# Performance work log

Measured on AMD Instinct MI355X. Metric: run time of the kernel, lower is better.

Reference implementation:

```python
import jax, jax.numpy as jnp
from jax import lax
import numpy as np
import math

B, C, Hs, Ws = 2, 512, 48, 48
HW = Hs * Ws            # 2304; also m (compress_ratio = 1)
M = HW
GROUPS = 256
GS = M // GROUPS        # 9, exact split
ALPHA = 0.05
MAXITER = 43
TOL = B * HW * 1e-7     # torch: z0.numel()*tol with z0 of shape [N, HW]
EPS = 1e-5
POWER_ITERS = 100


def _make_A():
    # random projection: num_ones = round(sqrt(m)) ones per column, rows L2-normalized
    rng = np.random.RandomState(0)
    num_ones = int(round(math.sqrt(M)))  # 48
    A = np.zeros((M, HW), dtype=np.float32)
    rows = np.argsort(rng.rand(HW, M), axis=1)[:, :num_ones]  # [HW, num_ones]
    A[rows.ravel(), np.repeat(np.arange(HW), num_ones)] = 1.0
    A /= np.maximum(np.sqrt((A ** 2).sum(axis=1, keepdims=True)), 1e-12)
    return jnp.asarray(A)


def setup_inputs() -> dict:
    key = jax.random.key(0)
    ks = jax.random.split(key, 10)
    f32 = jnp.float32
    d = {
        'content': jax.random.normal(ks[0], (B, C, Hs, Ws), f32),
        'style': jax.random.normal(ks[1], (B, C, Hs, Ws), f32),
        'content_key': jax.random.normal(ks[2], (B, C, Hs, Ws), f32),
        'style_key': jax.random.normal(ks[3], (B, C, Hs, Ws), f32),
        'f_w': jax.random.normal(ks[4], (C, C), f32) * 0.02,
        'f_b': jnp.zeros((C,), f32),
        'g_w': jax.random.normal(ks[5], (C, C), f32) * 0.02,
        'g_b': jnp.zeros((C,), f32),
        'h_w': jax.random.normal(ks[6], (C, C), f32) * 0.02,
        'h_b': jnp.zeros((C,), f32),
        'A': _make_A(),
    }
    return d


def _conv1x1(x, w, b):
    # nn.Conv2d(Cin, Cout, 1): [b,c,h,w] x [o,c] + bias
    return jnp.einsum('bchw,oc->bohw', x, w) + b[None, :, None, None]


def _softshrink(x, lam):
    return jnp.sign(x) * jnp.maximum(jnp.abs(x) - lam, 0.0)


def _forward(content, style, content_key, style_key, f_w, f_b, g_w, g_b, h_w, h_b, A):
    Fq = _conv1x1(content_key, f_w, f_b).reshape(B, C, HW).transpose(0, 2, 1)  # [b,HWc,Ck]
    G = _conv1x1(style_key, g_w, g_b).reshape(B, C, HW)                        # [b,Ck,HWs]
    Hh = _conv1x1(style, h_w, h_b).reshape(B, C, HW)
    # HW <= max_sample: no subsampling branch
    style_flat = Hh.transpose(0, 2, 1)                                         # [b,HWs,C]
    S = jax.nn.softmax(jnp.einsum('bqc,bck->bqk', Fq, G), axis=-1)             # [b,HWc,HWs]
    mean = jnp.einsum('bqk,bkc->bqc', S, style_flat)                           # weighted mean
    std = jnp.sqrt(jax.nn.relu(jnp.einsum('bqk,bkc->bqc', S, style_flat ** 2) - mean ** 2))
    mean = mean.transpose(0, 2, 1)  # [b,C,HW]
    std = std.transpose(0, 2, 1)
    # random projection along spatial dim: feat @ A^T
    proj = lambda f: jnp.einsum('mh,bch->bcm', A, f)
    mean_c = proj(mean)
    std_c = proj(std)
    cont_c = proj(content.reshape(B, C, HW))
    # per-group mean/variance norm (256 equal groups of GS along compressed dim)
    g = cont_c.reshape(B, C, GROUPS, GS)
    mu = g.mean(axis=-1, keepdims=True)
    var = g.var(axis=-1, ddof=1, keepdims=True)  # torch var is unbiased
    normed = (g - mu) / jnp.sqrt(var + EPS)
    x = (normed * std_c.reshape(B, C, GROUPS, GS)
         + mean_c.reshape(B, C, GROUPS, GS)).reshape(B, C, M)
    # FISTA sparse coding: min 0.5||z A^T - x||^2 + alpha |z|_1
    Ad = lax.stop_gradient(A)
    WtW = Ad.T @ Ad
    v = jnp.full((HW,), 1.0 / math.sqrt(HW), jnp.float32)
    def _pi(v, _):
        w = WtW @ v
        return w / jnp.linalg.norm(w), None
    v, _ = lax.scan(_pi, v, None, length=POWER_ITERS)
    L = v @ (WtW @ v)  # largest eigenvalue of A^T A
    lr = 1.0 / L
    z0 = jnp.zeros((B, C, HW), x.dtype)

    def step(carry, _):
        z, y, t, done = carry
        resid = jnp.einsum('bch,mh->bcm', y, A) - x   # y @ A^T - x
        grad = jnp.einsum('bcm,mh->bch', resid, A)    # resid @ A
        zn = _softshrink(y - lr * grad, ALPHA * lr)
        diff = jnp.abs(z - zn).sum()
        tn = (1.0 + jnp.sqrt(1.0 + 4.0 * t * t)) / 2.0
        yn = zn + (t - 1.0) / tn * (zn - z)
        z2 = jnp.where(done, z, zn)
        y2 = jnp.where(done, y, yn)
        t2 = jnp.where(done, t, tn)
        done2 = done | (diff <= TOL)
        return (z2, y2, t2, done2), None

    (z, _, _, _), _ = lax.scan(step, (z0, z0, jnp.float32(1.0), jnp.array(False)),
                               None, length=MAXITER)
    return z.reshape(B, C, Hs, Ws)


def reference(content, style, content_key, style_key, f_w, f_b, g_w, g_b, h_w, h_b, A):
    return _forward(content, style, content_key, style_key,
                    f_w, f_b, g_w, g_b, h_w, h_b, A)
```

## Files before the change

kernel.cpp:

```cpp
#include <hip/hip_runtime.h>
#include <hip/hip_cooperative_groups.h>
#include <math.h>

namespace cg = cooperative_groups;

#define TPB 256

typedef _Float16 f16;
typedef _Float16 half8 __attribute__((ext_vector_type(8)));
typedef _Float16 f16x2 __attribute__((ext_vector_type(2)));
typedef _Float16 f16x4 __attribute__((ext_vector_type(4)));
typedef float floatx4 __attribute__((ext_vector_type(4)));

static constexpr int CDIM = 512;
static constexpr int HWD = 2304;
static constexpr float ALPHA = 0.05f;
static constexpr float TOLF = 4.608e-4f;

enum { EPI_F32 = 0, EPI_F16BIASN = 1, EPI_F16BIASM = 2, EPI_F16 = 3,
       EPI_WTW = 4, EPI_MEANSTD = 5 };

__device__ __forceinline__ bool fista_done(const float* __restrict__ diffArr, int iter) {
    bool done = false;
    for (int j = 0; j < iter; ++j) done = done || (diffArr[j] <= TOLF);
    return done;
}

__device__ __forceinline__ void gload_lds(const f16* g, f16* l) {
#if __has_builtin(__builtin_amdgcn_global_load_lds)
    __builtin_amdgcn_global_load_lds(
        (__attribute__((address_space(1))) void*)(g),
        (__attribute__((address_space(3))) void*)(l), 16, 0, 0);
#else
    *(int4*)l = *(const int4*)g;
#endif
}

template<int N> __device__ __forceinline__ void vwait() {
    if constexpr (N == 0)      asm volatile("s_waitcnt vmcnt(0)" ::: "memory");
    else if constexpr (N == 4) asm volatile("s_waitcnt vmcnt(4)" ::: "memory");
    else if constexpr (N == 6) asm volatile("s_waitcnt vmcnt(6)" ::: "memory");
}

__device__ __forceinline__ void barrier_f() {
    asm volatile("" ::: "memory");
    __builtin_amdgcn_s_barrier();
    asm volatile("" ::: "memory");
}

template<int EPI, int MF>
__global__ __launch_bounds__(TPB, 4) void sgemm(
    const f16* __restrict__ A, long a_bs, int lda,
    const f16* __restrict__ B, long b_bs, int ldb,
    void* __restrict__ C0, long c_bs, int ldc,
    void* __restrict__ C1,
    int K,
    const float* __restrict__ bias)
{
    constexpr int ASZ = MF * 32 * 64;
    constexpr int BSZ = 64 * 64;
    constexpr int LCNT = MF + 2;
    __shared__ alignas(16) f16 As[2 * ASZ];
    __shared__ alignas(16) f16 Bs[2 * BSZ];
    const int tid = threadIdx.x;
    const int wid = tid >> 6, lane = tid & 63;
    const int wr = wid >> 1, wc = wid & 1;

    const int gx = gridDim.x, gy = gridDim.y;
    const int nwg = gx * gy;
    const int d = blockIdx.y * gx + blockIdx.x;
    const int q = nwg >> 3, r = nwg & 7;
    const int xcd = d & 7, rest = d >> 3;
    const int wgid = (xcd < r ? xcd * (q + 1) : r * (q + 1) + (xcd - r) * q) + rest;
    const int bx = wgid / gy, by = wgid % gy;

    const int m0 = by * (MF * 32), n0 = bx << 6;
    const f16* Ab = A + (long)blockIdx.z * a_bs;
    const f16* Bb = B + (long)blockIdx.z * b_bs;

    floatx4 acc[MF][2] = {};
    floatx4 acc2[MF][2] = {};

    const int rl = lane & 15, kg = lane >> 4;
    const int lrow = lane >> 3;
    const int gs = (lane & 7) ^ lrow;
    const int nt = K >> 6;

    auto STAGE = [&](int t, int buf) {
        const long k0 = (long)t << 6;
        f16* Ad = As + buf * ASZ;
        f16* Bd = Bs + buf * BSZ;
        #pragma unroll
        for (int p = 0; p < MF; ++p) {
            const int c = wid * MF + p;
            const int R = c * 8 + lrow;
            gload_lds(Ab + (long)(m0 + R) * lda + k0 + gs * 8, Ad + c * 512);
        }
        #pragma unroll
        for (int p = 0; p < 2; ++p) {
            const int c = wid * 2 + p;
            const int R = c * 8 + lrow;
            gload_lds(Bb + (long)(n0 + R) * ldb + k0 + gs * 8, Bd + c * 512);
        }
    };

    STAGE(0, 0);
    for (int t = 0; t < nt; ++t) {
        if (t + 1 < nt) { STAGE(t + 1, (t + 1) & 1); vwait<LCNT>(); }
        else            { vwait<0>(); }
        barrier_f();
        const f16* Ac = As + (t & 1) * ASZ;
        const f16* Bc = Bs + (t & 1) * BSZ;
        #pragma unroll
        for (int kk = 0; kk < 2; ++kk) {
            const int j = kk * 4 + kg;
            half8 af[MF], bf[2];
            #pragma unroll
            for (int f = 0; f < MF; ++f) {
                const int rowa = wr * (MF * 16) + f * 16 + rl;
                af[f] = *(const half8*)&Ac[rowa * 64 + ((j ^ (rowa & 7)) * 8)];
            }
            #pragma unroll
            for (int f = 0; f < 2; ++f) {
                const int rowb = wc * 32 + f * 16 + rl;
                bf[f] = *(const half8*)&Bc[rowb * 64 + ((j ^ (rowb & 7)) * 8)];
            }
            #pragma unroll
            for (int fi = 0; fi < MF; ++fi) {
                #pragma unroll
                for (int fj = 0; fj < 2; ++fj) {
                    acc[fi][fj] = __builtin_amdgcn_mfma_f32_16x16x32_f16(af[fi], bf[fj], acc[fi][fj], 0, 0, 0);
                    if constexpr (EPI == EPI_MEANSTD) {
                        half8 bq = bf[fj] * bf[fj];
                        acc2[fi][fj] = __builtin_amdgcn_mfma_f32_16x16x32_f16(af[fi], bq, acc2[fi][fj], 0, 0, 0);
                    }
                }
            }
        }
        barrier_f();
    }

    const int rg = lane >> 4;
    const int bz = blockIdx.z;
    #pragma unroll
    for (int fi = 0; fi < MF; ++fi) {
        #pragma unroll
        for (int fj = 0; fj < 2; ++fj) {
            #pragma unroll
            for (int r2 = 0; r2 < 4; ++r2) {
                const int row = m0 + wr * (MF * 16) + fi * 16 + rg * 4 + r2;
                const int col = n0 + wc * 32 + fj * 16 + rl;
                const float v = acc[fi][fj][r2];
                if constexpr (EPI == EPI_F32) {
                    ((float*)C0)[bz * c_bs + (long)row * ldc + col] = v;
                } else if constexpr (EPI == EPI_F16BIASN) {
                    ((f16*)C0)[bz * c_bs + (long)row * ldc + col] = (f16)(v + bias[col]);
                } else if constexpr (EPI == EPI_F16BIASM) {
                    ((f16*)C0)[bz * c_bs + (long)row * ldc + col] = (f16)(v + bias[row]);
                } else if constexpr (EPI == EPI_F16) {
                    ((f16*)C0)[bz * c_bs + (long)row * ldc + col] = (f16)v;
                } else if constexpr (EPI == EPI_WTW) {
                    ((float*)C0)[(long)row * ldc + col] = v;
                    ((f16*)C1)[(long)row * ldc + col] = (f16)v;
                } else if constexpr (EPI == EPI_MEANSTD) {
                    const float m_ = v;
                    float s2 = acc2[fi][fj][r2] - m_ * m_;
                    const long o = ((long)bz * CDIM + col) * HWD + row;
                    ((f16*)C0)[o] = (f16)m_;
                    ((f16*)C1)[o] = (f16)sqrtf(s2 > 0.f ? s2 : 0.f);
                }
            }
        }
    }
}

__global__ __launch_bounds__(TPB, 3) void fista_fast(
    const f16* __restrict__ Wh,
    const float* __restrict__ xAf,
    f16* __restrict__ yA, f16* __restrict__ yB,
    const float* __restrict__ lrs,
    unsigned int* __restrict__ cnt,
    int* __restrict__ flag,
    float* __restrict__ dout)
{
    constexpr int MF = 2;
    constexpr int ASZ = MF * 32 * 64;
    constexpr int BSZ = 64 * 64;
    constexpr int LCNT = MF + 2;
    __shared__ alignas(16) f16 As[2 * ASZ];
    __shared__ alignas(16) f16 Bs[2 * BSZ];
    __shared__ float red[TPB];
    const int tid = threadIdx.x;
    const int wid = tid >> 6, lane = tid & 63;
    const int wr = wid >> 1, wc = wid & 1;

    const int d = blockIdx.x;
    const int g = d & 15;
    const int ntile = d >> 4;
    const int m0 = g << 6, n0 = ntile << 6;

    const int rl = lane & 15, kg = lane >> 4;
    const int rg = lane >> 4;
    const int lrow = lane >> 3;
    const int gs = (lane & 7) ^ lrow;
    constexpr int nt = HWD >> 6;

    const float lr = lrs[0], sh = lrs[1];

    float xar[MF][2][4], zr[MF][2][4], yr[MF][2][4];
    #pragma unroll
    for (int fi = 0; fi < MF; ++fi)
        #pragma unroll
        for (int fj = 0; fj < 2; ++fj)
            #pragma unroll
            for (int r2 = 0; r2 < 4; ++r2) {
                const int row = m0 + wr * (MF * 16) + fi * 16 + rg * 4 + r2;
                const int col = n0 + wc * 32 + fj * 16 + rl;
                xar[fi][fj][r2] = xAf[(long)row * HWD + col];
                zr[fi][fj][r2] = 0.f;
                yr[fi][fj][r2] = 0.f;
            }

    float t = 1.0f;
    for (int iter = 0; iter < 43; ++iter) {
        const float tn = (1.0f + sqrtf(1.0f + 4.0f * t * t)) * 0.5f;
        const float coef = (t - 1.0f) / tn;
        t = tn;
        const f16* Yin = (iter & 1) ? yB : yA;
        f16* Yout = (iter & 1) ? yA : yB;

        floatx4 acc[MF][2] = {};
        auto STAGE = [&](int tt, int buf) {
            const long k0 = (long)tt << 6;
            f16* Ad = As + buf * ASZ;
            f16* Bd = Bs + buf * BSZ;
            #pragma unroll
            for (int p = 0; p < MF; ++p) {
                const int c = wid * MF + p;
                const int R = c * 8 + lrow;
                gload_lds(Yin + (long)(m0 + R) * HWD + k0 + gs * 8, Ad + c * 512);
            }
            #pragma unroll
            for (int p = 0; p < 2; ++p) {
                const int c = wid * 2 + p;
                const int R = c * 8 + lrow;
                gload_lds(Wh + (long)(n0 + R) * HWD + k0 + gs * 8, Bd + c * 512);
            }
        };
        STAGE(0, 0);
        for (int tt = 0; tt < nt; ++tt) {
            if (tt + 1 < nt) { STAGE(tt + 1, (tt + 1) & 1); vwait<LCNT>(); }
            else             { vwait<0>(); }
            barrier_f();
            const f16* Ac = As + (tt & 1) * ASZ;
            const f16* Bc = Bs + (tt & 1) * BSZ;
            #pragma unroll
            for (int kk = 0; kk < 2; ++kk) {
                const int j = kk * 4 + kg;
                half8 af[MF], bf[2];
                #pragma unroll
                for (int f = 0; f < MF; ++f) {
                    const int rowa = wr * (MF * 16) + f * 16 + rl;
                    af[f] = *(const half8*)&Ac[rowa * 64 + ((j ^ (rowa & 7)) * 8)];
                }
                #pragma unroll
                for (int f = 0; f < 2; ++f) {
                    const int rowb = wc * 32 + f * 16 + rl;
                    bf[f] = *(const half8*)&Bc[rowb * 64 + ((j ^ (rowb & 7)) * 8)];
                }
                #pragma unroll
                for (int fi = 0; fi < MF; ++fi)
                    #pragma unroll
                    for (int fj = 0; fj < 2; ++fj)
                        acc[fi][fj] = __builtin_amdgcn_mfma_f32_16x16x32_f16(af[fi], bf[fj], acc[fi][fj], 0, 0, 0);
            }
            barrier_f();
        }

        float loc = 0.f;
        #pragma unroll
        for (int fi = 0; fi < MF; ++fi)
            #pragma unroll
            for (int fj = 0; fj < 2; ++fj)
                #pragma unroll
                for (int r2 = 0; r2 < 4; ++r2) {
                    const int row = m0 + wr * (MF * 16) + fi * 16 + rg * 4 + r2;
                    const int col = n0 + wc * 32 + fj * 16 + rl;
                    const float grad = acc[fi][fj][r2] - xar[fi][fj][r2];
                    const float p = yr[fi][fj][r2] - lr * grad;
                    const float ap = fabsf(p) - sh;
                    const float zn = ap > 0.f ? copysignf(ap, p) : 0.f;
                    const float zo = zr[fi][fj][r2];
                    loc += fabsf(zn - zo);
                    const float yn = zn + coef * (zn - zo);
                    zr[fi][fj][r2] = zn;
                    yr[fi][fj][r2] = yn;
                    Yout[(long)row * HWD + col] = (f16)yn;
                }
        red[tid] = loc; __syncthreads();
        for (int s = 128; s > 0; s >>= 1) { if (tid < s) red[tid] += red[tid + s]; __syncthreads(); }
        if (tid == 0 && red[0] <= TOLF)
            __hip_atomic_store(flag, 1, __ATOMIC_RELEASE, __HIP_MEMORY_SCOPE_AGENT);

        __threadfence();
        __syncthreads();
        if (tid == 0) {
            __hip_atomic_fetch_add(&cnt[g], 1u, __ATOMIC_RELEASE, __HIP_MEMORY_SCOPE_AGENT);
            const unsigned int need = 36u * (unsigned int)(iter + 1);
            while (__hip_atomic_load(&cnt[g], __ATOMIC_ACQUIRE, __HIP_MEMORY_SCOPE_AGENT) < need)
                __builtin_amdgcn_s_sleep(2);
        }
        __syncthreads();
        __threadfence();
    }

    #pragma unroll
    for (int fi = 0; fi < MF; ++fi)
        #pragma unroll
        for (int fj = 0; fj < 2; ++fj)
            #pragma unroll
            for (int r2 = 0; r2 < 4; ++r2) {
                const int row = m0 + wr * (MF * 16) + fi * 16 + rg * 4 + r2;
                const int col = n0 + wc * 32 + fj * 16 + rl;
                dout[(long)row * HWD + col] = zr[fi][fj][r2];
            }
}

__global__ __launch_bounds__(TPB, 2) void fista_coop(
    const f16* __restrict__ Wh,
    const float* __restrict__ xAf,
    f16* __restrict__ yA, f16* __restrict__ yB,
    const float* __restrict__ lrs,
    float* __restrict__ diffArr,
    const int* __restrict__ flag,
    float* __restrict__ dout)
{
    if (__hip_atomic_load(flag, __ATOMIC_ACQUIRE, __HIP_MEMORY_SCOPE_AGENT) == 0) return;
    cg::grid_group grid = cg::this_grid();
    constexpr int MF = 4;
    constexpr int ASZ = MF * 32 * 64;
    constexpr int BSZ = 64 * 64;
    constexpr int LCNT = MF + 2;
    __shared__ alignas(16) f16 As[2 * ASZ];
    __shared__ alignas(16) f16 Bs[2 * BSZ];
    __shared__ float red[TPB];
    const int tid = threadIdx.x;
    const int wid = tid >> 6, lane = tid & 63;
    const int wr = wid >> 1, wc = wid & 1;

    const int d = blockIdx.x;
    const int wgid = (d & 7) * 36 + (d >> 3);
    const int bx = wgid >> 3, by = wgid & 7;
    const int m0 = by << 7, n0 = bx << 6;

    const int rl = lane & 15, kg = lane >> 4;
    const int rg = lane >> 4;
    const int lrow = lane >> 3;
    const int gs = (lane & 7) ^ lrow;
    constexpr int nt = HWD >> 6;

    const float lr = lrs[0], sh = lrs[1];

    float xar[MF][2][4], zr[MF][2][4], yr[MF][2][4];
    #pragma unroll
    for (int fi = 0; fi < MF; ++fi)
        #pragma unroll
        for (int fj = 0; fj < 2; ++fj)
            #pragma unroll
            for (int r2 = 0; r2 < 4; ++r2) {
                const int row = m0 + wr * (MF * 16) + fi * 16 + rg * 4 + r2;
                const int col = n0 + wc * 32 + fj * 16 + rl;
                xar[fi][fj][r2] = xAf[(long)row * HWD + col];
                zr[fi][fj][r2] = 0.f;
                yr[fi][fj][r2] = 0.f;
            }

    float t = 1.0f;
    for (int iter = 0; iter < 43; ++iter) {
        const float tn = (1.0f + sqrtf(1.0f + 4.0f * t * t)) * 0.5f;
        const float coef = (t - 1.0f) / tn;
        t = tn;
        const f16* Yin = (iter & 1) ? yB : yA;
        f16* Yout = (iter & 1) ? yA : yB;

        floatx4 acc[MF][2] = {};
        auto STAGE = [&](int tt, int buf) {
            const long k0 = (long)tt << 6;
            f16* Ad = As + buf * ASZ;
            f16* Bd = Bs + buf * BSZ;
            #pragma unroll
            for (int p = 0; p < MF; ++p) {
                const int c = wid * MF + p;
                const int R = c * 8 + lrow;
                gload_lds(Yin + (long)(m0 + R) * HWD + k0 + gs * 8, Ad + c * 512);
            }
            #pragma unroll
            for (int p = 0; p < 2; ++p) {
                const int c = wid * 2 + p;
                const int R = c * 8 + lrow;
                gload_lds(Wh + (long)(n0 + R) * HWD + k0 + gs * 8, Bd + c * 512);
            }
        };
        STAGE(0, 0);
        for (int tt = 0; tt < nt; ++tt) {
            if (tt + 1 < nt) { STAGE(tt + 1, (tt + 1) & 1); vwait<LCNT>(); }
            else             { vwait<0>(); }
            barrier_f();
            const f16* Ac = As + (tt & 1) * ASZ;
            const f16* Bc = Bs + (tt & 1) * BSZ;
            #pragma unroll
            for (int kk = 0; kk < 2; ++kk) {
                const int j = kk * 4 + kg;
                half8 af[MF], bf[2];
                #pragma unroll
                for (int f = 0; f < MF; ++f) {
                    const int rowa = wr * (MF * 16) + f * 16 + rl;
                    af[f] = *(const half8*)&Ac[rowa * 64 + ((j ^ (rowa & 7)) * 8)];
                }
                #pragma unroll
                for (int f = 0; f < 2; ++f) {
                    const int rowb = wc * 32 + f * 16 + rl;
                    bf[f] = *(const half8*)&Bc[rowb * 64 + ((j ^ (rowb & 7)) * 8)];
                }
                #pragma unroll
                for (int fi = 0; fi < MF; ++fi)
                    #pragma unroll
                    for (int fj = 0; fj < 2; ++fj)
                        acc[fi][fj] = __builtin_amdgcn_mfma_f32_16x16x32_f16(af[fi], bf[fj], acc[fi][fj], 0, 0, 0);
            }
            barrier_f();
        }

        float loc = 0.f;
        #pragma unroll
        for (int fi = 0; fi < MF; ++fi)
            #pragma unroll
            for (int fj = 0; fj < 2; ++fj)
                #pragma unroll
                for (int r2 = 0; r2 < 4; ++r2) {
                    const int row = m0 + wr * (MF * 16) + fi * 16 + rg * 4 + r2;
                    const int col = n0 + wc * 32 + fj * 16 + rl;
                    const float grad = acc[fi][fj][r2] - xar[fi][fj][r2];
                    const float p = yr[fi][fj][r2] - lr * grad;
                    const float ap = fabsf(p) - sh;
                    const float zn = ap > 0.f ? copysignf(ap, p) : 0.f;
                    const float zo = zr[fi][fj][r2];
                    loc += fabsf(zn - zo);
                    const float yn = zn + coef * (zn - zo);
                    zr[fi][fj][r2] = zn;
                    yr[fi][fj][r2] = yn;
                    Yout[(long)row * HWD + col] = (f16)yn;
                }
        red[tid] = loc; __syncthreads();
        for (int s = 128; s > 0; s >>= 1) { if (tid < s) red[tid] += red[tid + s]; __syncthreads(); }
        if (tid == 0) atomicAdd(&diffArr[iter], red[0]);

        __threadfence();
        grid.sync();
        __threadfence();
        const float dsum = __hip_atomic_load(&diffArr[iter], __ATOMIC_RELAXED,
                                             __HIP_MEMORY_SCOPE_AGENT);
        if (dsum <= TOLF) break;
    }

    #pragma unroll
    for (int fi = 0; fi < MF; ++fi)
        #pragma unroll
        for (int fj = 0; fj < 2; ++fj)
            #pragma unroll
            for (int r2 = 0; r2 < 4; ++r2) {
                const int row = m0 + wr * (MF * 16) + fi * 16 + rg * 4 + r2;
                const int col = n0 + wc * 32 + fj * 16 + rl;
                dout[(long)row * HWD + col] = zr[fi][fj][r2];
            }
}

__global__ __launch_bounds__(TPB, 3) void fista_step(
    const f16* __restrict__ Yin, const f16* __restrict__ Wh,
    const float* __restrict__ xAf,
    float* __restrict__ zc, float* __restrict__ zp, f16* __restrict__ yhp,
    const float* __restrict__ lrs, float coefPrev, float coefCur,
    float* __restrict__ diffArr, int iter)
{
    if (iter > 0 && fista_done(diffArr, iter)) return;
    constexpr int MF = 2;
    constexpr int ASZ = MF * 32 * 64;
    constexpr int BSZ = 64 * 64;
    constexpr int LCNT = MF + 2;
    __shared__ alignas(16) f16 As[2 * ASZ];
    __shared__ alignas(16) f16 Bs[2 * BSZ];
    __shared__ float red[TPB];
    const int tid = threadIdx.x;
    const int wid = tid >> 6, lane = tid & 63;
    const int wr = wid >> 1, wc = wid & 1;

    const int d = blockIdx.y * gridDim.x + blockIdx.x;
    const int wgid = (d & 7) * 72 + (d >> 3);
    const int bx = wgid >> 4, by = wgid & 15;
    const int m0 = by << 6, n0 = bx << 6;

    floatx4 acc[MF][2] = {};
    const int rl = lane & 15, kg = lane >> 4;
    const int lrow = lane >> 3;
    const int gs = (lane & 7) ^ lrow;
    constexpr int nt = HWD >> 6;

    auto STAGE = [&](int t, int buf) {
        const long k0 = (long)t << 6;
        f16* Ad = As + buf * ASZ;
        f16* Bd = Bs + buf * BSZ;
        #pragma unroll
        for (int p = 0; p < MF; ++p) {
            const int c = wid * MF + p;
            const int R = c * 8 + lrow;
            gload_lds(Yin + (long)(m0 + R) * HWD + k0 + gs * 8, Ad + c * 512);
        }
        #pragma unroll
        for (int p = 0; p < 2; ++p) {
            const int c = wid * 2 + p;
            const int R = c * 8 + lrow;
            gload_lds(Wh + (long)(n0 + R) * HWD + k0 + gs * 8, Bd + c * 512);
        }
    };
    STAGE(0, 0);
    for (int t = 0; t < nt; ++t) {
        if (t + 1 < nt) { STAGE(t + 1, (t + 1) & 1); vwait<LCNT>(); }
        else            { vwait<0>(); }
        barrier_f();
        const f16* Ac = As + (t & 1) * ASZ;
        const f16* Bc = Bs + (t & 1) * BSZ;
        #pragma unroll
        for (int kk = 0; kk < 2; ++kk) {
            const int j = kk * 4 + kg;
            half8 af[MF], bf[2];
            #pragma unroll
            for (int f = 0; f < MF; ++f) {
                const int rowa = wr * (MF * 16) + f * 16 + rl;
                af[f] = *(const half8*)&Ac[rowa * 64 + ((j ^ (rowa & 7)) * 8)];
            }
            #pragma unroll
            for (int f = 0; f < 2; ++f) {
                const int rowb = wc * 32 + f * 16 + rl;
                bf[f] = *(const half8*)&Bc[rowb * 64 + ((j ^ (rowb & 7)) * 8)];
            }
            #pragma unroll
            for (int fi = 0; fi < MF; ++fi)
                #pragma unroll
                for (int fj = 0; fj < 2; ++fj)
                    acc[fi][fj] = __builtin_amdgcn_mfma_f32_16x16x32_f16(af[fi], bf[fj], acc[fi][fj], 0, 0, 0);
        }
        barrier_f();
    }

    const int rg = lane >> 4;
    const float lr = lrs[0], sh = lrs[1];
    float loc = 0.f;
    #pragma unroll
    for (int fi = 0; fi < MF; ++fi)
        #pragma unroll
        for (int fj = 0; fj < 2; ++fj)
            #pragma unroll
            for (int r2 = 0; r2 < 4; ++r2) {
                const int row = m0 + wr * (MF * 16) + fi * 16 + rg * 4 + r2;
                const int col = n0 + wc * 32 + fj * 16 + rl;
                const long off = (long)row * HWD + col;
                const float zk = zc[off];
                const float zkm = zp[off];
                const float ykf = zk + coefPrev * (zk - zkm);
                const float grad = acc[fi][fj][r2] - xAf[off];
                const float p = ykf - lr * grad;
                const float ap = fabsf(p) - sh;
                const float zn = ap > 0.f ? copysignf(ap, p) : 0.f;
                zp[off] = zn;
                yhp[off] = (f16)(zn + coefCur * (zn - zk));
                loc += fabsf(zn - zk);
            }
    red[tid] = loc; __syncthreads();
    for (int s = 128; s > 0; s >>= 1) { if (tid < s) red[tid] += red[tid + s]; __syncthreads(); }
    if (tid == 0) atomicAdd(&diffArr[iter], red[0]);
}

__global__ __launch_bounds__(TPB) void tcvt(const float* __restrict__ in, long in_bs,
                                            f16* __restrict__ out, long out_bs, int R, int Cc) {
    __shared__ float t[32][33];
    const int b = blockIdx.z;
    const int r0 = blockIdx.y << 5, c0 = blockIdx.x << 5;
    const int tx = threadIdx.x & 31, ty = threadIdx.x >> 5;
    const float* ib = in + (long)b * in_bs;
    #pragma unroll
    for (int p = 0; p < 4; ++p) {
        const int r = ty + p * 8;
        t[r][tx] = ib[(long)(r0 + r) * Cc + c0 + tx];
    }
    __syncthreads();
    f16* ob = out + (long)b * out_bs;
    #pragma unroll
    for (int p = 0; p < 4; ++p) {
        const int c = ty + p * 8;
        ob[(long)(c0 + c) * R + r0 + tx] = (f16)t[tx][c];
    }
}

__global__ void cvt16(const float4* __restrict__ in, f16x4* __restrict__ out, long n4) {
    long i = (long)blockIdx.x * blockDim.x + threadIdx.x;
    const long st = (long)gridDim.x * blockDim.x;
    for (; i < n4; i += st) {
        const float4 v = in[i];
        f16x4 o; o.x = (f16)v.x; o.y = (f16)v.y; o.z = (f16)v.z; o.w = (f16)v.w;
        out[i] = o;
    }
}

__global__ __launch_bounds__(TPB) void softmax_h(const float* __restrict__ Sf, f16* __restrict__ Sh) {
    __shared__ float row[HWD];
    __shared__ float red[TPB];
    const long base = (long)blockIdx.x * HWD;
    const int tid = threadIdx.x;
    float mx = -3.4e38f;
    for (int i = tid; i < HWD; i += TPB) { const float v = Sf[base + i]; row[i] = v; mx = fmaxf(mx, v); }
    red[tid] = mx; __syncthreads();
    for (int s = 128; s > 0; s >>= 1) { if (tid < s) red[tid] = fmaxf(red[tid], red[tid + s]); __syncthreads(); }
    mx = red[0]; __syncthreads();
    float sum = 0.f;
    for (int i = tid; i < HWD; i += TPB) { const float e = expf(row[i] - mx); row[i] = e; sum += e; }
    red[tid] = sum; __syncthreads();
    for (int s = 128; s > 0; s >>= 1) { if (tid < s) red[tid] += red[tid + s]; __syncthreads(); }
    const float inv = 1.0f / red[0];
    for (int i = tid; i < HWD; i += TPB) Sh[base + i] = (f16)(row[i] * inv);
}

__global__ __launch_bounds__(TPB) void groupnorm_x(const float* __restrict__ contc,
                                                   const float* __restrict__ meanc,
                                                   const float* __restrict__ stdc,
                                                   f16* __restrict__ xh) {
    const long base = (long)blockIdx.x * HWD + (long)threadIdx.x * 9;
    float v[9];
    float mu = 0.f;
    #pragma unroll
    for (int j = 0; j < 9; ++j) { v[j] = contc[base + j]; mu += v[j]; }
    mu *= (1.0f / 9.0f);
    float var = 0.f;
    #pragma unroll
    for (int j = 0; j < 9; ++j) { const float d = v[j] - mu; var += d * d; }
    var *= (1.0f / 8.0f);
    const float rs = 1.0f / sqrtf(var + 1e-5f);
    #pragma unroll
    for (int j = 0; j < 9; ++j)
        xh[base + j] = (f16)((v[j] - mu) * rs * (float)stdc[base + j] + (float)meanc[base + j]);
}

__global__ __launch_bounds__(TPB) void matvec_h(const f16* __restrict__ Wm,
                                                const float* __restrict__ win,
                                                float* __restrict__ wout) {
    __shared__ float red[TPB];
    const int tid = threadIdx.x;
    float s = 0.f;
    for (int i = tid; i < HWD; i += TPB) { const float v = win[i]; s += v * v; }
    red[tid] = s; __syncthreads();
    for (int st = 128; st > 0; st >>= 1) { if (tid < st) red[tid] += red[tid + st]; __syncthreads(); }
    const float ninv = rsqrtf(red[0]);
    const int row = (blockIdx.x << 2) + (tid >> 6);
    const int lane = tid & 63;
    const f16x2* wr2 = (const f16x2*)(Wm + (long)row * HWD);
    float d = 0.f;
    for (int j = lane; j < HWD / 2; j += 64) {
        const f16x2 p = wr2[j];
        d += (float)p.x * win[2 * j] + (float)p.y * win[2 * j + 1];
    }
    #pragma unroll
    for (int o = 32; o > 0; o >>= 1) d += __shfl_down(d, o);
    if (lane == 0) wout[row] = d * ninv;
}

__global__ __launch_bounds__(TPB) void kernelL(const float* __restrict__ Wf,
                                               const float* __restrict__ w,
                                               float* __restrict__ Lnum, float* __restrict__ Lden) {
    __shared__ float red[TPB];
    const int tid = threadIdx.x;
    const int row = (blockIdx.x << 2) + (tid >> 6);
    const int lane = tid & 63;
    const float* wr = Wf + (long)row * HWD;
    float d = 0.f;
    for (int j = lane; j < HWD; j += 64) d += wr[j] * w[j];
    #pragma unroll
    for (int o = 32; o > 0; o >>= 1) d += __shfl_down(d, o);
    red[tid] = (lane == 0) ? d * w[row] : 0.f;
    __syncthreads();
    for (int s = 128; s > 0; s >>= 1) { if (tid < s) red[tid] += red[tid + s]; __syncthreads(); }
    if (tid == 0) atomicAdd(Lnum, red[0]);
    if (blockIdx.x == 0) {
        __syncthreads();
        float s2 = 0.f;
        for (int i = tid; i < HWD; i += TPB) { const float v = w[i]; s2 += v * v; }
        red[tid] = s2; __syncthreads();
        for (int s = 128; s > 0; s >>= 1) { if (tid < s) red[tid] += red[tid + s]; __syncthreads(); }
        if (tid == 0) *Lden = red[0];
    }
}

__global__ void lr_fin(const float* __restrict__ Lnum, const float* __restrict__ Lden,
                       float* __restrict__ lrs) {
    const float lr = Lden[0] / Lnum[0];
    lrs[0] = lr;
    lrs[1] = ALPHA * lr;
}

__global__ void init_small(float* __restrict__ wvec, float* __restrict__ diffArr,
                           float* __restrict__ Lnum, unsigned int* __restrict__ cnt,
                           int* __restrict__ flag) {
    const int tid = threadIdx.x;
    for (int i = tid; i < HWD; i += TPB) wvec[i] = (float)(1.0 / 48.0);
    if (tid < 43) diffArr[tid] = 0.f;
    if (tid == 64) Lnum[0] = 0.f;
    if (tid >= 80 && tid < 96) cnt[tid - 80] = 0u;
    if (tid == 96) *flag = 0;
}

__global__ void zero_kernel(float4* __restrict__ p, long n4) {
    long i = (long)blockIdx.x * blockDim.x + threadIdx.x;
    const long st = (long)gridDim.x * blockDim.x;
    for (; i < n4; i += st) p[i] = make_float4(0.f, 0.f, 0.f, 0.f);
}

__global__ void zero_if(const int* __restrict__ flag, float4* __restrict__ p, long n4) {
    if (__hip_atomic_load(flag, __ATOMIC_ACQUIRE, __HIP_MEMORY_SCOPE_AGENT) == 0) return;
    long i = (long)blockIdx.x * blockDim.x + threadIdx.x;
    const long st = (long)gridDim.x * blockDim.x;
    for (; i < n4; i += st) p[i] = make_float4(0.f, 0.f, 0.f, 0.f);
}

__global__ void copy_fista(const float4* __restrict__ zfA, const float4* __restrict__ zfB,
                           float4* __restrict__ out, const float* __restrict__ diffArr, long n4) {
    int last = 42;
    for (int j = 0; j < 43; ++j) { if (diffArr[j] <= TOLF) { last = j; break; } }
    const float4* src = (last & 1) ? zfA : zfB;
    long i = (long)blockIdx.x * blockDim.x + threadIdx.x;
    const long st = (long)gridDim.x * blockDim.x;
    for (; i < n4; i += st) out[i] = src[i];
}

extern "C" void kernel_launch(void* const* d_in, const int* in_sizes, int n_in,
                              void* d_out, int out_size, void* d_ws, size_t ws_size,
                              hipStream_t stream) {
    (void)in_sizes; (void)n_in; (void)out_size;
    const float* content = (const float*)d_in[0];
    const float* style   = (const float*)d_in[1];
    const float* ckey    = (const float*)d_in[2];
    const float* skey    = (const float*)d_in[3];
    const float* f_w = (const float*)d_in[4];
    const float* f_b = (const float*)d_in[5];
    const float* g_w = (const float*)d_in[6];
    const float* g_b = (const float*)d_in[7];
    const float* h_w = (const float*)d_in[8];
    const float* h_b = (const float*)d_in[9];
    const float* Amat = (const float*)d_in[10];

    if (ws_size < 79500000) return;
    char* W = (char*)d_ws;

    const long E16 = (long)HWD * CDIM;
    const long EHH = (long)HWD * HWD;
    f16*  ckeyT = (f16*)(W + 0);
    f16*  skeyT = (f16*)(W + 4718592);
    f16*  styleT= (f16*)(W + 9437184);
    float* Sf   = (float*)(W + 0);
    f16*  Ah    = (f16*)(W + 0);
    f16*  At    = (f16*)(W + 10616832);
    f16*  Wh    = (f16*)(W + 21233664);
    f16*  W4h   = (f16*)(W + 31850496);
    f16*  W2h   = (f16*)(W + 0);
    float* contc= (float*)(W + 21233664);
    float* zfA  = (float*)(W + 0);
    float* zfB  = (float*)(W + 9437184);
    f16*  yhA   = (f16*)(W + 31850496);
    f16*  yhB   = (f16*)(W + 36569088);
    f16*  Sh    = (f16*)(W + 42467328);
    float* meanc= (float*)(W + 42467328);
    float* stdc = (float*)(W + 42467328 + 9437184);
    float* Wf   = (float*)(W + 42467328);
    float* xAf  = (float*)(W + 42467328);
    f16*  Fh    = (f16*)(W + 63700992);
    f16*  Gh    = (f16*)(W + 63700992 + 4718592);
    f16*  Hh    = (f16*)(W + 63700992 + 9437184);
    f16*  meanx = (f16*)(W + 63700992);
    f16*  stdx  = (f16*)(W + 63700992 + 4718592);
    f16*  conth = (f16*)(W + 63700992 + 9437184);
    f16*  xh    = (f16*)(W + 63700992);
    float* w_a  = (float*)(W + 77856768);
    float* w_b  = (float*)(W + 77856768 + 9216);
    float* lrs  = (float*)(W + 77856768 + 18432);
    float* Lnum = (float*)(W + 77856768 + 18440);
    float* Lden = (float*)(W + 77856768 + 18444);
    float* diffArr = (float*)(W + 77856768 + 18448);
    unsigned int* cnt = (unsigned int*)(W + 77856768 + 18624);
    int*  flag  = (int*)(W + 77856768 + 18688);
    f16*  fwh   = (f16*)(W + 77875712);
    f16*  gwh   = (f16*)(W + 77875712 + 524288);
    f16*  hwh   = (f16*)(W + 77875712 + 1048576);

    init_small<<<1, TPB, 0, stream>>>(w_a, diffArr, Lnum, cnt, flag);

    cvt16<<<256, TPB, 0, stream>>>((const float4*)f_w, (f16x4*)fwh, (long)CDIM * CDIM / 4);
    cvt16<<<256, TPB, 0, stream>>>((const float4*)g_w, (f16x4*)gwh, (long)CDIM * CDIM / 4);
    cvt16<<<256, TPB, 0, stream>>>((const float4*)h_w, (f16x4*)hwh, (long)CDIM * CDIM / 4);
    tcvt<<<dim3(72, 16, 2), TPB, 0, stream>>>(ckey, E16, ckeyT, E16, CDIM, HWD);
    tcvt<<<dim3(72, 16, 2), TPB, 0, stream>>>(skey, E16, skeyT, E16, CDIM, HWD);
    tcvt<<<dim3(72, 16, 2), TPB, 0, stream>>>(style, E16, styleT, E16, CDIM, HWD);

    sgemm<EPI_F16BIASN, 2><<<dim3(8, 36, 2), TPB, 0, stream>>>(ckeyT, E16, CDIM, fwh, 0, CDIM,
        Fh, E16, CDIM, nullptr, CDIM, f_b);
    sgemm<EPI_F16BIASN, 2><<<dim3(8, 36, 2), TPB, 0, stream>>>(skeyT, E16, CDIM, gwh, 0, CDIM,
        Gh, E16, CDIM, nullptr, CDIM, g_b);
    sgemm<EPI_F16BIASM, 2><<<dim3(36, 8, 2), TPB, 0, stream>>>(hwh, 0, CDIM, styleT, E16, CDIM,
        Hh, E16, HWD, nullptr, CDIM, h_b);

    sgemm<EPI_F32, 2><<<dim3(36, 36, 2), TPB, 0, stream>>>(Fh, E16, CDIM, Gh, E16, CDIM,
        Sf, EHH, HWD, nullptr, CDIM, nullptr);
    softmax_h<<<2 * HWD, TPB, 0, stream>>>(Sf, Sh);

    cvt16<<<2048, TPB, 0, stream>>>((const float4*)Amat, (f16x4*)Ah, EHH / 4);
    tcvt<<<dim3(72, 72, 1), TPB, 0, stream>>>(Amat, 0, At, 0, HWD, HWD);

    sgemm<EPI_MEANSTD, 2><<<dim3(8, 36, 2), TPB, 0, stream>>>(Sh, EHH, HWD, Hh, E16, HWD,
        meanx, 0, HWD, stdx, HWD, nullptr);

    cvt16<<<2048, TPB, 0, stream>>>((const float4*)content, (f16x4*)conth, (long)2 * E16 / 4);

    sgemm<EPI_F32, 2><<<dim3(36, 16, 1), TPB, 0, stream>>>(meanx, 0, HWD, Ah, 0, HWD,
        meanc, 0, HWD, nullptr, HWD, nullptr);
    sgemm<EPI_F32, 2><<<dim3(36, 16, 1), TPB, 0, stream>>>(stdx, 0, HWD, Ah, 0, HWD,
        stdc, 0, HWD, nullptr, HWD, nullptr);
    sgemm<EPI_F32, 2><<<dim3(36, 16, 1), TPB, 0, stream>>>(conth, 0, HWD, Ah, 0, HWD,
        contc, 0, HWD, nullptr, HWD, nullptr);

    groupnorm_x<<<1024, TPB, 0, stream>>>(contc, meanc, stdc, xh);

    sgemm<EPI_WTW, 2><<<dim3(36, 36, 1), TPB, 0, stream>>>(At, 0, HWD, At, 0, HWD,
        Wf, 0, HWD, Wh, HWD, nullptr);
    sgemm<EPI_F16, 2><<<dim3(36, 36, 1), TPB, 0, stream>>>(Wh, 0, HWD, Wh, 0, HWD,
        W2h, 0, HWD, nullptr, HWD, nullptr);
    sgemm<EPI_F16, 2><<<dim3(36, 36, 1), TPB, 0, stream>>>(W2h, 0, HWD, W2h, 0, HWD,
        W4h, 0, HWD, nullptr, HWD, nullptr);

    for (int it = 0; it < 25; ++it) {
        const float* win = (it & 1) ? w_b : w_a;
        float* wout = (it & 1) ? w_a : w_b;
        matvec_h<<<HWD / 4, TPB, 0, stream>>>(W4h, win, wout);
    }
    kernelL<<<HWD / 4, TPB, 0, stream>>>(Wf, w_b, Lnum, Lden);
    lr_fin<<<1, 1, 0, stream>>>(Lnum, Lden, lrs);

    sgemm<EPI_F32, 2><<<dim3(36, 16, 1), TPB, 0, stream>>>(xh, 0, HWD, At, 0, HWD,
        xAf, 0, HWD, nullptr, HWD, nullptr);

    int dev = 0; hipGetDevice(&dev);
    int coopOK = 0, numCU = 0, maxFast = 0, maxCoop = 0;
    hipDeviceGetAttribute(&coopOK, hipDeviceAttributeCooperativeLaunch, dev);
    hipDeviceGetAttribute(&numCU, hipDeviceAttributeMultiprocessorCount, dev);
    hipOccupancyMaxActiveBlocksPerMultiprocessor(&maxFast, fista_fast, TPB, 0);
    hipOccupancyMaxActiveBlocksPerMultiprocessor(&maxCoop, fista_coop, TPB, 0);
    const bool usePersist = coopOK && ((long)maxFast * numCU >= 576)
                                   && ((long)maxCoop * numCU >= 288);

    zero_kernel<<<1024, TPB, 0, stream>>>((float4*)yhA, E16 / 4);

    if (usePersist) {
        float* doutF = (float*)d_out;
        {
            void* args[] = { (void*)&Wh, (void*)&xAf, (void*)&yhA, (void*)&yhB,
                             (void*)&lrs, (void*)&cnt, (void*)&flag, (void*)&doutF };
            hipLaunchCooperativeKernel((const void*)fista_fast, dim3(576), dim3(TPB),
                                       args, 0, stream);
        }
        zero_if<<<1024, TPB, 0, stream>>>(flag, (float4*)yhA, E16 / 4);
        {
            void* args[] = { (void*)&Wh, (void*)&xAf, (void*)&yhA, (void*)&yhB,
                             (void*)&lrs, (void*)&diffArr, (void*)&flag, (void*)&doutF };
            hipLaunchCooperativeKernel((const void*)fista_coop, dim3(288), dim3(TPB),
                                       args, 0, stream);
        }
    } else {
        zero_kernel<<<1024, TPB, 0, stream>>>((float4*)zfA, E16);
        float t = 1.0f, coefPrev = 0.0f;
        for (int it = 0; it < 43; ++it) {
            const float tn = (1.0f + sqrtf(1.0f + 4.0f * t * t)) * 0.5f;
            const float coef = (t - 1.0f) / tn;
            t = tn;
            float* zc = (it & 1) ? zfB : zfA;
            float* zp = (it & 1) ? zfA : zfB;
            fista_step<<<dim3(36, 16, 1), TPB, 0, stream>>>(yhA, Wh, xAf, zc, zp, yhA,
                                                            lrs, coefPrev, coef, diffArr, it);
            coefPrev = coef;
        }
        copy_fista<<<2048, TPB, 0, stream>>>((const float4*)zfA, (const float4*)zfB,
                                             (float4*)d_out, diffArr, 2 * E16 / 4);
    }
}
```

Baseline: 2.123 ms.

## Drop device-wide fences in FISTA group barrier, relying on same-XCD L2 coherence

Removes the __threadfence calls around the per-group barrier in the persistent FISTA kernel. Y loads now use an AUX cache-policy bit so they bypass the per-CU cache, and the spin wait after the first iteration uses relaxed loads. Correctness now depends on all blocks of a group sharing one XCD's L2. On the first iteration each group records the XCC IDs of its blocks and sets the fallback flag if they span more than one. This cuts fence and cache-invalidation cost on each of the 43 iterations, but relies on the hardware placing blocks per XCD and on the flag-driven fallback path.

```diff
diff --git a/kernel.cpp b/kernel.cpp
--- a/kernel.cpp
+++ b/kernel.cpp
@@ -26,11 +26,12 @@
     return done;
 }
 
+template<int AUX>
 __device__ __forceinline__ void gload_lds(const f16* g, f16* l) {
 #if __has_builtin(__builtin_amdgcn_global_load_lds)
     __builtin_amdgcn_global_load_lds(
         (__attribute__((address_space(1))) void*)(g),
-        (__attribute__((address_space(3))) void*)(l), 16, 0, 0);
+        (__attribute__((address_space(3))) void*)(l), 16, 0, AUX);
 #else
     *(int4*)l = *(const int4*)g;
 #endif
@@ -94,13 +95,13 @@
         for (int p = 0; p < MF; ++p) {
             const int c = wid * MF + p;
             const int R = c * 8 + lrow;
-            gload_lds(Ab + (long)(m0 + R) * lda + k0 + gs * 8, Ad + c * 512);
+            gload_lds<0>(Ab + (long)(m0 + R) * lda + k0 + gs * 8, Ad + c * 512);
         }
         #pragma unroll
         for (int p = 0; p < 2; ++p) {
             const int c = wid * 2 + p;
             const int R = c * 8 + lrow;
-            gload_lds(Bb + (long)(n0 + R) * ldb + k0 + gs * 8, Bd + c * 512);
+            gload_lds<0>(Bb + (long)(n0 + R) * ldb + k0 + gs * 8, Bd + c * 512);
         }
     };
 
@@ -180,6 +181,7 @@
     f16* __restrict__ yA, f16* __restrict__ yB,
     const float* __restrict__ lrs,
     unsigned int* __restrict__ cnt,
+    unsigned int* __restrict__ xcdmask,
     int* __restrict__ flag,
     float* __restrict__ dout)
 {
@@ -199,6 +201,10 @@
     const int ntile = d >> 4;
     const int m0 = g << 6, n0 = ntile << 6;
 
+    unsigned int myxcd;
+    asm volatile("s_getreg_b32 %0, hwreg(HW_REG_XCC_ID)" : "=s"(myxcd));
+    myxcd &= 7u;
+
     const int rl = lane & 15, kg = lane >> 4;
     const int rg = lane >> 4;
     const int lrow = lane >> 3;
@@ -238,13 +244,13 @@
             for (int p = 0; p < MF; ++p) {
                 const int c = wid * MF + p;
                 const int R = c * 8 + lrow;
-                gload_lds(Yin + (long)(m0 + R) * HWD + k0 + gs * 8, Ad + c * 512);
+                gload_lds<1>(Yin + (long)(m0 + R) * HWD + k0 + gs * 8, Ad + c * 512);
             }
             #pragma unroll
             for (int p = 0; p < 2; ++p) {
                 const int c = wid * 2 + p;
                 const int R = c * 8 + lrow;
-                gload_lds(Wh + (long)(n0 + R) * HWD + k0 + gs * 8, Bd + c * 512);
+                gload_lds<0>(Wh + (long)(n0 + R) * HWD + k0 + gs * 8, Bd + c * 512);
             }
         };
         STAGE(0, 0);
@@ -302,16 +308,26 @@
         if (tid == 0 && red[0] <= TOLF)
             __hip_atomic_store(flag, 1, __ATOMIC_RELEASE, __HIP_MEMORY_SCOPE_AGENT);
 
-        __threadfence();
         __syncthreads();
         if (tid == 0) {
+            if (iter == 0)
+                __hip_atomic_fetch_or(&xcdmask[g], 1u << myxcd,
+                                      __ATOMIC_RELEASE, __HIP_MEMORY_SCOPE_AGENT);
             __hip_atomic_fetch_add(&cnt[g], 1u, __ATOMIC_RELEASE, __HIP_MEMORY_SCOPE_AGENT);
             const unsigned int need = 36u * (unsigned int)(iter + 1);
-            while (__hip_atomic_load(&cnt[g], __ATOMIC_ACQUIRE, __HIP_MEMORY_SCOPE_AGENT) < need)
-                __builtin_amdgcn_s_sleep(2);
+            if (iter == 0) {
+                while (__hip_atomic_load(&cnt[g], __ATOMIC_ACQUIRE, __HIP_MEMORY_SCOPE_AGENT) < need)
+                    __builtin_amdgcn_s_sleep(2);
+                const unsigned int m = __hip_atomic_load(&xcdmask[g], __ATOMIC_RELAXED,
+                                                         __HIP_MEMORY_SCOPE_AGENT);
+                if (__builtin_popcount(m) != 1)
+                    __hip_atomic_store(flag, 1, __ATOMIC_RELEASE, __HIP_MEMORY_SCOPE_AGENT);
+            } else {
+                while (__hip_atomic_load(&cnt[g], __ATOMIC_RELAXED, __HIP_MEMORY_SCOPE_AGENT) < need)
+                    __builtin_amdgcn_s_sleep(2);
+            }
         }
         __syncthreads();
-        __threadfence();
     }
 
     #pragma unroll
@@ -392,13 +408,13 @@
             for (int p = 0; p < MF; ++p) {
                 const int c = wid * MF + p;
                 const int R = c * 8 + lrow;
-                gload_lds(Yin + (long)(m0 + R) * HWD + k0 + gs * 8, Ad + c * 512);
+                gload_lds<0>(Yin + (long)(m0 + R) * HWD + k0 + gs * 8, Ad + c * 512);
             }
             #pragma unroll
             for (int p = 0; p < 2; ++p) {
                 const int c = wid * 2 + p;
                 const int R = c * 8 + lrow;
-                gload_lds(Wh + (long)(n0 + R) * HWD + k0 + gs * 8, Bd + c * 512);
+                gload_lds<0>(Wh + (long)(n0 + R) * HWD + k0 + gs * 8, Bd + c * 512);
             }
         };
         STAGE(0, 0);
@@ -513,13 +529,13 @@
         for (int p = 0; p < MF; ++p) {
             const int c = wid * MF + p;
             const int R = c * 8 + lrow;
-            gload_lds(Yin + (long)(m0 + R) * HWD + k0 + gs * 8, Ad + c * 512);
+            gload_lds<0>(Yin + (long)(m0 + R) * HWD + k0 + gs * 8, Ad + c * 512);
         }
         #pragma unroll
         for (int p = 0; p < 2; ++p) {
             const int c = wid * 2 + p;
             const int R = c * 8 + lrow;
-            gload_lds(Wh + (long)(n0 + R) * HWD + k0 + gs * 8, Bd + c * 512);
+            gload_lds<0>(Wh + (long)(n0 + R) * HWD + k0 + gs * 8, Bd + c * 512);
         }
     };
     STAGE(0, 0);
@@ -707,13 +723,14 @@
 
 __global__ void init_small(float* __restrict__ wvec, float* __restrict__ diffArr,
                            float* __restrict__ Lnum, unsigned int* __restrict__ cnt,
-                           int* __restrict__ flag) {
+                           unsigned int* __restrict__ xcdmask, int* __restrict__ flag) {
     const int tid = threadIdx.x;
     for (int i = tid; i < HWD; i += TPB) wvec[i] = (float)(1.0 / 48.0);
     if (tid < 43) diffArr[tid] = 0.f;
     if (tid == 64) Lnum[0] = 0.f;
     if (tid >= 80 && tid < 96) cnt[tid - 80] = 0u;
-    if (tid == 96) *flag = 0;
+    if (tid >= 96 && tid < 112) xcdmask[tid - 96] = 0u;
+    if (tid == 112) *flag = 0;
 }
 
 __global__ void zero_kernel(float4* __restrict__ p, long n4) {
@@ -793,12 +810,13 @@
     float* Lden = (float*)(W + 77856768 + 18444);
     float* diffArr = (float*)(W + 77856768 + 18448);
     unsigned int* cnt = (unsigned int*)(W + 77856768 + 18624);
-    int*  flag  = (int*)(W + 77856768 + 18688);
+    unsigned int* xcdmask = (unsigned int*)(W + 77856768 + 18688);
+    int*  flag  = (int*)(W + 77856768 + 18752);
     f16*  fwh   = (f16*)(W + 77875712);
     f16*  gwh   = (f16*)(W + 77875712 + 524288);
     f16*  hwh   = (f16*)(W + 77875712 + 1048576);
 
-    init_small<<<1, TPB, 0, stream>>>(w_a, diffArr, Lnum, cnt, flag);
+    init_small<<<1, TPB, 0, stream>>>(w_a, diffArr, Lnum, cnt, xcdmask, flag);
 
     cvt16<<<256, TPB, 0, stream>>>((const float4*)f_w, (f16x4*)fwh, (long)CDIM * CDIM / 4);
     cvt16<<<256, TPB, 0, stream>>>((const float4*)g_w, (f16x4*)gwh, (long)CDIM * CDIM / 4);
@@ -868,7 +886,8 @@
         float* doutF = (float*)d_out;
         {
             void* args[] = { (void*)&Wh, (void*)&xAf, (void*)&yhA, (void*)&yhB,
-                             (void*)&lrs, (void*)&cnt, (void*)&flag, (void*)&doutF };
+                             (void*)&lrs, (void*)&cnt, (void*)&xcdmask, (void*)&flag,
+                             (void*)&doutF };
             hipLaunchCooperativeKernel((const void*)fista_fast, dim3(576), dim3(TPB),
                                        args, 0, stream);
         }
```

New measurement: 2.116 ms. About the same (-0.3%).
